# Optimization experiments

Measured on AMD Instinct MI355X. Metric: run time of the kernel, lower is better.

The kernel has to match this reference:

```python
import jax, jax.numpy as jnp
import numpy as np

B = 8192
D_IN = 1024
D_H = 1024


def _lin(x, w, b):
    # torch nn.Linear: y = x @ w.T + b, w: [out, in]
    return x @ w.T + b


def setup_inputs() -> dict:
    key = jax.random.key(0)
    ks = iter(jax.random.split(key, 64))
    s = 0.02

    def w(shape):
        return (jax.random.normal(next(ks), shape, dtype=jnp.float32) * s)

    inp = {
        "x": jax.random.normal(next(ks), (B, D_IN), dtype=jnp.float32),
        "h_prev": jax.random.normal(next(ks), (B, D_H), dtype=jnp.float32),
        "c_prev": jax.random.normal(next(ks), (B, D_H), dtype=jnp.float32),
    }
    for name in ["Wi", "Wf", "Wo", "Wc", "Ws"]:
        inp[name + "_w"] = w((D_H, D_IN))
        inp[name + "_b"] = w((D_H,))
    for name in ["Ui", "Uf", "Uo", "Uc", "Us"]:
        inp[name + "_w"] = w((D_H, D_H))
        inp[name + "_b"] = w((D_H,))
    # alpha_mlp: Linear(in+h -> h), ReLU, Linear(h -> 1), Sigmoid
    inp["a1_w"] = w((D_H, D_IN + D_H)); inp["a1_b"] = w((D_H,))
    inp["a2_w"] = w((1, D_H)); inp["a2_b"] = w((1,))
    inp["r1_w"] = w((D_H, D_H)); inp["r1_b"] = w((D_H,))
    inp["r2_w"] = w((D_H, D_H)); inp["r2_b"] = w((D_H,))
    inp["r3_w"] = w((D_H, D_H)); inp["r3_b"] = w((D_H,))
    return inp


def reference(x, h_prev, c_prev,
              Wi_w, Wi_b, Wf_w, Wf_b, Wo_w, Wo_b, Wc_w, Wc_b, Ws_w, Ws_b,
              Ui_w, Ui_b, Uf_w, Uf_b, Uo_w, Uo_b, Uc_w, Uc_b, Us_w, Us_b,
              a1_w, a1_b, a2_w, a2_b,
              r1_w, r1_b, r2_w, r2_b, r3_w, r3_b):
    i_t = jax.nn.sigmoid(_lin(x, Wi_w, Wi_b) + _lin(h_prev, Ui_w, Ui_b))
    f_t = jax.nn.sigmoid(_lin(x, Wf_w, Wf_b) + _lin(h_prev, Uf_w, Uf_b))
    o_t = jax.nn.sigmoid(_lin(x, Wo_w, Wo_b) + _lin(h_prev, Uo_w, Uo_b))
    c_hat_t = jnp.tanh(_lin(x, Wc_w, Wc_b) + _lin(h_prev, Uc_w, Uc_b))

    combined = jnp.concatenate([x, h_prev], axis=-1)  # [B, D_IN + D_H]
    alpha_t = jax.nn.sigmoid(_lin(jax.nn.relu(_lin(combined, a1_w, a1_b)), a2_w, a2_b))  # [B, 1]

    s_t = jax.nn.sigmoid(_lin(x, Ws_w, Ws_b) + _lin(h_prev, Us_w, Us_b))

    c_t = f_t * c_prev + i_t * c_hat_t * s_t * alpha_t

    residual = _lin(jax.nn.relu(_lin(jax.nn.relu(_lin(h_prev, r1_w, r1_b)), r2_w, r2_b)), r3_w, r3_b)
    c_t = c_t + residual
    h_t = o_t * jnp.tanh(c_t)
    return (h_t, c_t)
```

## Files before the change

### kernel.cpp

```cpp
#include <hip/hip_runtime.h>
#include <hip/hip_bf16.h>

typedef __bf16 bf16;
typedef __bf16 bf16x8 __attribute__((ext_vector_type(8)));
typedef __bf16 bf16x4 __attribute__((ext_vector_type(4)));
typedef float f32x4 __attribute__((ext_vector_type(4)));

#define NBIG 7168
#define KBIG 2048

__device__ __forceinline__ float sigmoid_f(float x) { return 1.0f / (1.0f + __expf(-x)); }
__device__ __forceinline__ float tanh_f(float x) { return 1.0f - 2.0f / (__expf(2.0f * x) + 1.0f); }

__device__ __forceinline__ void gload_lds16(const bf16* g, bf16* lds) {
  __builtin_amdgcn_global_load_lds(
      (const __attribute__((address_space(1))) unsigned int*)g,
      (__attribute__((address_space(3))) unsigned int*)lds,
      16, 0, 0);
}


__global__ __launch_bounds__(256) void build_A(const float* __restrict__ x,
                                               const float* __restrict__ h,
                                               bf16* __restrict__ A) {
  const int i4 = blockIdx.x * 256 + threadIdx.x;
  const int o = i4 * 4;
  const int m = o >> 11;
  const int c = o & 2047;
  const float4 v = (c < 1024) ? *(const float4*)&x[(size_t)m * 1024 + c]
                              : *(const float4*)&h[(size_t)m * 1024 + (c - 1024)];
  bf16x4 b;
  b[0] = (bf16)v.x; b[1] = (bf16)v.y; b[2] = (bf16)v.z; b[3] = (bf16)v.w;
  *(bf16x4*)&A[(size_t)o] = b;
}

__global__ __launch_bounds__(256) void build_WG(
    const float* __restrict__ Wi, const float* __restrict__ Wf, const float* __restrict__ Wo,
    const float* __restrict__ Wc, const float* __restrict__ Ws,
    const float* __restrict__ Ui, const float* __restrict__ Uf, const float* __restrict__ Uo,
    const float* __restrict__ Uc, const float* __restrict__ Us,
    const float* __restrict__ a1w, const float* __restrict__ r1w, bf16* __restrict__ WG) {
  const int i4 = blockIdx.x * 256 + threadIdx.x;
  const int o = i4 * 4;
  const int n = o >> 11;
  const int c = o & 2047;
  const int g = n >> 10;
  const int r = n & 1023;
  float4 v;
  if (g < 5) {
    const float* Wp = g == 0 ? Wi : g == 1 ? Wf : g == 2 ? Wo : g == 3 ? Wc : Ws;
    const float* Up = g == 0 ? Ui : g == 1 ? Uf : g == 2 ? Uo : g == 3 ? Uc : Us;
    v = (c < 1024) ? *(const float4*)&Wp[(size_t)r * 1024 + c]
                   : *(const float4*)&Up[(size_t)r * 1024 + (c - 1024)];
  } else if (g == 5) {
    v = *(const float4*)&a1w[(size_t)r * 2048 + c];
  } else {
    if (c < 1024) { v.x = 0.f; v.y = 0.f; v.z = 0.f; v.w = 0.f; }
    else v = *(const float4*)&r1w[(size_t)r * 1024 + (c - 1024)];
  }
  bf16x4 b;
  b[0] = (bf16)v.x; b[1] = (bf16)v.y; b[2] = (bf16)v.z; b[3] = (bf16)v.w;
  *(bf16x4*)&WG[(size_t)o] = b;
}

__global__ __launch_bounds__(256) void build_bias(
    const float* __restrict__ Wib, const float* __restrict__ Wfb, const float* __restrict__ Wob,
    const float* __restrict__ Wcb, const float* __restrict__ Wsb,
    const float* __restrict__ Uib, const float* __restrict__ Ufb, const float* __restrict__ Uob,
    const float* __restrict__ Ucb, const float* __restrict__ Usb,
    const float* __restrict__ a1b, const float* __restrict__ r1b, float* __restrict__ bias) {
  const int n = blockIdx.x * 256 + threadIdx.x;
  if (n >= NBIG) return;
  const int g = n >> 10, r = n & 1023;
  float v;
  if (g < 5) {
    const float* Wb = g == 0 ? Wib : g == 1 ? Wfb : g == 2 ? Wob : g == 3 ? Wcb : Wsb;
    const float* Ub = g == 0 ? Uib : g == 1 ? Ufb : g == 2 ? Uob : g == 3 ? Ucb : Usb;
    v = Wb[r] + Ub[r];
  } else if (g == 5) v = a1b[r];
  else v = r1b[r];
  bias[n] = v;
}

__global__ __launch_bounds__(256) void f2b(const float* __restrict__ s, bf16* __restrict__ d,
                                           int n4) {
  const int i = blockIdx.x * 256 + threadIdx.x;
  if (i >= n4) return;
  const float4 v = *(const float4*)&s[(size_t)i * 4];
  bf16x4 b;
  b[0] = (bf16)v.x; b[1] = (bf16)v.y; b[2] = (bf16)v.z; b[3] = (bf16)v.w;
  *(bf16x4*)&d[(size_t)i * 4] = b;
}

__global__ __launch_bounds__(256) void gemm_bt(const bf16* __restrict__ A, int lda,
                                               const bf16* __restrict__ W, int K,
                                               const float* __restrict__ bias,
                                               bf16* __restrict__ C, int ldc, int act_mode) {
  __shared__ __align__(16) bf16 As[128 * 32];
  __shared__ __align__(16) bf16 Bs[128 * 32];

  const int tid = threadIdx.x;
  const int lane = tid & 63;
  const int wv = tid >> 6;
  const int bm = blockIdx.x * 128;
  const int bn = blockIdx.y * 128;
  const int wr = wv >> 1, wc = wv & 1;

  const int srow = wv * 16 + (lane >> 2);
  const int scol = (lane & 3) * 8;
  const bf16* ag0 = A + (size_t)(bm + srow) * lda + scol;
  const bf16* ag1 = ag0 + (size_t)64 * lda;
  const bf16* bg0 = W + (size_t)(bn + srow) * K + scol;
  const bf16* bg1 = bg0 + (size_t)64 * K;
  bf16* const al0 = &As[(wv * 16) * 32];
  bf16* const al1 = &As[(64 + wv * 16) * 32];
  bf16* const bl0 = &Bs[(wv * 16) * 32];
  bf16* const bl1 = &Bs[(64 + wv * 16) * 32];

  f32x4 acc[4][4] = {};

  const int k0 = (lane >> 4) * 8;
  const int fr = lane & 15;
  const int niter = K >> 5;
  for (int kt = 0; kt < niter; ++kt) {
    __syncthreads();
    gload_lds16(ag0, al0);
    gload_lds16(ag1, al1);
    gload_lds16(bg0, bl0);
    gload_lds16(bg1, bl1);
    ag0 += 32; ag1 += 32; bg0 += 32; bg1 += 32;
    __syncthreads();

    bf16x8 af[4], bfv[4];
#pragma unroll
    for (int f = 0; f < 4; ++f) {
      af[f] = *(const bf16x8*)&As[(wr * 64 + f * 16 + fr) * 32 + k0];
      bfv[f] = *(const bf16x8*)&Bs[(wc * 64 + f * 16 + fr) * 32 + k0];
    }
#pragma unroll
    for (int i = 0; i < 4; ++i)
#pragma unroll
      for (int j = 0; j < 4; ++j)
        acc[i][j] = __builtin_amdgcn_mfma_f32_16x16x32_bf16(af[i], bfv[j], acc[i][j], 0, 0, 0);
  }

  const int rbase = (lane >> 4) * 4;
#pragma unroll
  for (int j = 0; j < 4; ++j) {
    const int n = bn + wc * 64 + j * 16 + fr;
    const float bv = bias[n];
    const int g = (act_mode == 0) ? (n >> 10) : (act_mode == 1 ? 100 : 101);
#pragma unroll
    for (int i = 0; i < 4; ++i) {
      const size_t mrow = (size_t)(bm + wr * 64 + i * 16 + rbase);
#pragma unroll
      for (int r = 0; r < 4; ++r) {
        float v = acc[i][j][r] + bv;
        if (g == 3) v = tanh_f(v);
        else if (g < 5) v = sigmoid_f(v);
        else if (g < 7 || g == 100) v = fmaxf(v, 0.0f);
        C[(mrow + r) * (size_t)ldc + n] = (bf16)v;
      }
    }
  }
}

__global__ __launch_bounds__(256) void alpha_k(const bf16* __restrict__ G,
                                               const float* __restrict__ a2w,
                                               const float* __restrict__ a2b,
                                               float* __restrict__ alpha) {
  const int m = blockIdx.x * 4 + (threadIdx.x >> 6);
  const int lane = threadIdx.x & 63;
  const bf16* row = G + (size_t)m * NBIG + 5120 + lane * 16;
  const bf16x8 v0 = *(const bf16x8*)row;
  const bf16x8 v1 = *(const bf16x8*)(row + 8);
  const float* w = a2w + lane * 16;
  float s = 0.f;
#pragma unroll
  for (int e = 0; e < 8; ++e) s += (float)v0[e] * w[e] + (float)v1[e] * w[8 + e];
#pragma unroll
  for (int off = 32; off > 0; off >>= 1) s += __shfl_down(s, off, 64);
  if (lane == 0) alpha[m] = sigmoid_f(s + a2b[0]);
}

__global__ __launch_bounds__(256) void final_k(const bf16* __restrict__ G,
                                               const bf16* __restrict__ R3,
                                               const float* __restrict__ c_prev,
                                               const float* __restrict__ alpha,
                                               float* __restrict__ out) {
  const int idx = blockIdx.x * 256 + threadIdx.x;
  const int o = idx * 8;
  const int m = o >> 10;
  const int c = o & 1023;
  const size_t gb = (size_t)m * NBIG;
  const bf16x8 iv = *(const bf16x8*)&G[gb + c];
  const bf16x8 fv = *(const bf16x8*)&G[gb + 1024 + c];
  const bf16x8 ov = *(const bf16x8*)&G[gb + 2048 + c];
  const bf16x8 cv = *(const bf16x8*)&G[gb + 3072 + c];
  const bf16x8 sv = *(const bf16x8*)&G[gb + 4096 + c];
  const bf16x8 rv = *(const bf16x8*)&R3[(size_t)m * 1024 + c];
  const float al = alpha[m];
  const float* cp = &c_prev[(size_t)m * 1024 + c];
  float hbuf[8], cbuf[8];
#pragma unroll
  for (int e = 0; e < 8; ++e) {
    const float ct = (float)fv[e] * cp[e] + (float)iv[e] * (float)cv[e] * (float)sv[e] * al
                     + (float)rv[e];
    cbuf[e] = ct;
    hbuf[e] = (float)ov[e] * tanh_f(ct);
  }
  float* oh = out + (size_t)m * 1024 + c;
  float* oc = out + (size_t)8192 * 1024 + (size_t)m * 1024 + c;
#pragma unroll
  for (int e = 0; e < 8; ++e) { oh[e] = hbuf[e]; oc[e] = cbuf[e]; }
}

extern "C" void kernel_launch(void* const* d_in, const int* in_sizes, int n_in,
                              void* d_out, int out_size, void* d_ws, size_t ws_size,
                              hipStream_t stream) {
  const float* x      = (const float*)d_in[0];
  const float* h_prev = (const float*)d_in[1];
  const float* c_prev = (const float*)d_in[2];
  const float* Wi_w = (const float*)d_in[3];  const float* Wi_b = (const float*)d_in[4];
  const float* Wf_w = (const float*)d_in[5];  const float* Wf_b = (const float*)d_in[6];
  const float* Wo_w = (const float*)d_in[7];  const float* Wo_b = (const float*)d_in[8];
  const float* Wc_w = (const float*)d_in[9];  const float* Wc_b = (const float*)d_in[10];
  const float* Ws_w = (const float*)d_in[11]; const float* Ws_b = (const float*)d_in[12];
  const float* Ui_w = (const float*)d_in[13]; const float* Ui_b = (const float*)d_in[14];
  const float* Uf_w = (const float*)d_in[15]; const float* Uf_b = (const float*)d_in[16];
  const float* Uo_w = (const float*)d_in[17]; const float* Uo_b = (const float*)d_in[18];
  const float* Uc_w = (const float*)d_in[19]; const float* Uc_b = (const float*)d_in[20];
  const float* Us_w = (const float*)d_in[21]; const float* Us_b = (const float*)d_in[22];
  const float* a1_w = (const float*)d_in[23]; const float* a1_b = (const float*)d_in[24];
  const float* a2_w = (const float*)d_in[25]; const float* a2_b = (const float*)d_in[26];
  const float* r1_w = (const float*)d_in[27]; const float* r1_b = (const float*)d_in[28];
  const float* r2_w = (const float*)d_in[29]; const float* r2_b = (const float*)d_in[30];
  const float* r3_w = (const float*)d_in[31]; const float* r3_b = (const float*)d_in[32];

  char* ws = (char*)d_ws;
  size_t off = 0;
  auto alloc = [&](size_t bytes) -> void* {
    void* p = ws + off;
    off += (bytes + 255) & ~(size_t)255;
    return p;
  };
  bf16* A_big    = (bf16*)alloc((size_t)8192 * 2048 * 2);
  bf16* WG       = (bf16*)alloc((size_t)7168 * 2048 * 2);
  float* bias_bg = (float*)alloc((size_t)7168 * 4);
  bf16* WR2      = (bf16*)alloc((size_t)1024 * 1024 * 2);
  bf16* WR3      = (bf16*)alloc((size_t)1024 * 1024 * 2);
  bf16* G        = (bf16*)alloc((size_t)8192 * 7168 * 2);
  bf16* R2       = (bf16*)alloc((size_t)8192 * 1024 * 2);
  bf16* R3       = (bf16*)alloc((size_t)8192 * 1024 * 2);
  float* alpha   = (float*)alloc((size_t)8192 * 4);

  build_A<<<16384, 256, 0, stream>>>(x, h_prev, A_big);
  build_WG<<<14336, 256, 0, stream>>>(Wi_w, Wf_w, Wo_w, Wc_w, Ws_w,
                                      Ui_w, Uf_w, Uo_w, Uc_w, Us_w, a1_w, r1_w, WG);
  build_bias<<<28, 256, 0, stream>>>(Wi_b, Wf_b, Wo_b, Wc_b, Ws_b,
                                     Ui_b, Uf_b, Uo_b, Uc_b, Us_b, a1_b, r1_b, bias_bg);
  f2b<<<1024, 256, 0, stream>>>(r2_w, WR2, 262144);
  f2b<<<1024, 256, 0, stream>>>(r3_w, WR3, 262144);

  dim3 g1(64, 56);
  gemm_bt<<<g1, 256, 0, stream>>>(A_big, 2048, WG, 2048, bias_bg, G, NBIG, 0);

  alpha_k<<<2048, 256, 0, stream>>>(G, a2_w, a2_b, alpha);

  dim3 g2(64, 8);
  gemm_bt<<<g2, 256, 0, stream>>>(G + 6144, NBIG, WR2, 1024, r2_b, R2, 1024, 1);
  gemm_bt<<<g2, 256, 0, stream>>>(R2, 1024, WR3, 1024, r3_b, R3, 1024, 2);

  final_k<<<4096, 256, 0, stream>>>(G, R3, c_prev, alpha, (float*)d_out);
}
```

Measured before the change: 469.9 us.

## Replace big gate GEMM with 256x256 tiled, double-buffered, swizzled MFMA kernel

Measured after the change: 537.7 us. 14.4% more time.

```diff
diff --git a/kernel.cpp b/kernel.cpp
--- a/kernel.cpp
+++ b/kernel.cpp
@@ -92,6 +92,153 @@
   *(bf16x4*)&d[(size_t)i * 4] = b;
 }
 
+
+#define BAR __builtin_amdgcn_s_barrier()
+#define LGKM0 asm volatile("s_waitcnt lgkmcnt(0)" ::: "memory")
+#define VM4 asm volatile("s_waitcnt vmcnt(4)" ::: "memory")
+#define VM0 asm volatile("s_waitcnt vmcnt(0)" ::: "memory")
+#define PRIO1 __builtin_amdgcn_s_setprio(1)
+#define PRIO0 __builtin_amdgcn_s_setprio(0)
+
+__global__ __launch_bounds__(512, 2) void gemm256(
+    const bf16* __restrict__ A, int lda,
+    const bf16* __restrict__ W, int ldw, int K,
+    const float* __restrict__ bias,
+    bf16* __restrict__ C, int ldc, int act_mode, int mtiles) {
+  __shared__ __align__(16) bf16 sA[2][256 * 64];
+  __shared__ __align__(16) bf16 sB[2][256 * 64];
+
+  const int tid = threadIdx.x;
+  const int lane = tid & 63;
+  const int wv = tid >> 6;
+  const int wr = wv >> 2;
+  const int wc = wv & 3;
+
+  const int nwg = gridDim.x;
+  int wg = blockIdx.x;
+  if ((nwg & 7) == 0) wg = (wg & 7) * (nwg >> 3) + (wg >> 3);
+  const int bm = (wg % mtiles) * 256;
+  const int bn = (wg / mtiles) * 256;
+
+  const int srow = tid >> 3;
+  const int scole = ((tid & 7) ^ (srow & 7)) << 3;
+  const bf16* pA = A + (size_t)(bm + srow) * lda + scole;
+  const bf16* pB = W + (size_t)(bn + srow) * ldw + scole;
+
+  const int fr = lane & 15;
+  const int lg = lane >> 4;
+  const int swz = (lane & 7) << 4;
+
+  const int NT = K >> 6;
+
+  f32x4 acc[8][4] = {};
+  bf16x8 ar[4][2], br0[2][2], br1[2][2];
+
+#define STG_A(bb, hh, tt)                                          \
+  do {                                                             \
+    const bf16* g_ = pA + (size_t)((hh) * 128) * lda + (tt) * 64;  \
+    bf16* l_ = &sA[bb][((hh) * 128 + wv * 8) * 64];                \
+    gload_lds16(g_, l_);                                           \
+    gload_lds16(g_ + (size_t)64 * lda, l_ + 64 * 64);              \
+  } while (0)
+#define STG_B(bb, hh, tt)                                          \
+  do {                                                             \
+    const bf16* g_ = pB + (size_t)((hh) * 128) * ldw + (tt) * 64;  \
+    bf16* l_ = &sB[bb][((hh) * 128 + wv * 8) * 64];                \
+    gload_lds16(g_, l_);                                           \
+    gload_lds16(g_ + (size_t)64 * ldw, l_ + 64 * 64);              \
+  } while (0)
+#define LD_A(bb, mlo)                                                            \
+  do {                                                                           \
+    _Pragma("unroll") for (int mi = 0; mi < 4; ++mi)                             \
+    _Pragma("unroll") for (int kk = 0; kk < 2; ++kk)                             \
+        ar[mi][kk] = *(const bf16x8*)((const char*)&sA[bb][0] +                  \
+            (wr * 128 + ((mlo) + mi) * 16 + fr) * 128 +                          \
+            ((lg * 16 + kk * 64) ^ swz));                                        \
+  } while (0)
+#define LD_B(dst, bb, nlo)                                                       \
+  do {                                                                           \
+    _Pragma("unroll") for (int ni = 0; ni < 2; ++ni)                             \
+    _Pragma("unroll") for (int kk = 0; kk < 2; ++kk)                             \
+        dst[ni][kk] = *(const bf16x8*)((const char*)&sB[bb][0] +                 \
+            (wc * 64 + ((nlo) + ni) * 16 + fr) * 128 +                           \
+            ((lg * 16 + kk * 64) ^ swz));                                        \
+  } while (0)
+#define MM(mlo, nlo, br)                                                         \
+  do {                                                                           \
+    _Pragma("unroll") for (int mi = 0; mi < 4; ++mi)                             \
+    _Pragma("unroll") for (int ni = 0; ni < 2; ++ni) {                           \
+      acc[(mlo) + mi][(nlo) + ni] = __builtin_amdgcn_mfma_f32_16x16x32_bf16(     \
+          ar[mi][0], br[ni][0], acc[(mlo) + mi][(nlo) + ni], 0, 0, 0);           \
+      acc[(mlo) + mi][(nlo) + ni] = __builtin_amdgcn_mfma_f32_16x16x32_bf16(     \
+          ar[mi][1], br[ni][1], acc[(mlo) + mi][(nlo) + ni], 0, 0, 0);           \
+    }                                                                            \
+  } while (0)
+
+  STG_A(0, 0, 0); STG_A(0, 1, 0); STG_B(0, 0, 0); STG_B(0, 1, 0);
+  STG_B(1, 0, 1); STG_B(1, 1, 1);
+  VM4; BAR;
+
+  for (int t = 0; t + 3 < NT; t += 2) {
+    LD_A(0, 0); LD_B(br0, 0, 0); STG_A(1, 0, t + 1);
+    BAR; LGKM0; PRIO1; MM(0, 0, br0); PRIO0; BAR;
+    LD_B(br1, 0, 2); STG_A(1, 1, t + 1);
+    BAR; LGKM0; PRIO1; MM(0, 2, br1); PRIO0; BAR;
+    LD_A(0, 4); STG_B(0, 0, t + 2);
+    BAR; LGKM0; PRIO1; MM(4, 2, br1); PRIO0; BAR;
+    STG_B(0, 1, t + 2);
+    BAR; PRIO1; MM(4, 0, br0); PRIO0; VM4; BAR;
+    LD_A(1, 0); LD_B(br0, 1, 0); STG_A(0, 0, t + 2);
+    BAR; LGKM0; PRIO1; MM(0, 0, br0); PRIO0; BAR;
+    LD_B(br1, 1, 2); STG_A(0, 1, t + 2);
+    BAR; LGKM0; PRIO1; MM(0, 2, br1); PRIO0; BAR;
+    LD_A(1, 4); STG_B(1, 0, t + 3);
+    BAR; LGKM0; PRIO1; MM(4, 2, br1); PRIO0; BAR;
+    STG_B(1, 1, t + 3);
+    BAR; PRIO1; MM(4, 0, br0); PRIO0; VM4; BAR;
+  }
+
+  LD_A(0, 0); LD_B(br0, 0, 0); STG_A(1, 0, NT - 1);
+  BAR; LGKM0; PRIO1; MM(0, 0, br0); PRIO0; BAR;
+  LD_B(br1, 0, 2); STG_A(1, 1, NT - 1);
+  BAR; LGKM0; PRIO1; MM(0, 2, br1); PRIO0; BAR;
+  LD_A(0, 4);
+  BAR; LGKM0; PRIO1; MM(4, 2, br1); PRIO0; BAR;
+  PRIO1; MM(4, 0, br0); PRIO0; VM0; BAR;
+  LD_A(1, 0); LD_B(br0, 1, 0);
+  BAR; LGKM0; PRIO1; MM(0, 0, br0); PRIO0; BAR;
+  LD_B(br1, 1, 2);
+  BAR; LGKM0; PRIO1; MM(0, 2, br1); PRIO0; BAR;
+  LD_A(1, 4);
+  BAR; LGKM0; PRIO1; MM(4, 2, br1); PRIO0; BAR;
+  PRIO1; MM(4, 0, br0); PRIO0;
+
+  const int rbase = lg * 4;
+#pragma unroll
+  for (int j = 0; j < 4; ++j) {
+    const int n = bn + wc * 64 + j * 16 + fr;
+    const float bv = bias[n];
+    const int g = (act_mode == 0) ? (n >> 10) : (act_mode == 1 ? 100 : 101);
+#pragma unroll
+    for (int mi = 0; mi < 8; ++mi) {
+      const size_t mrow = (size_t)(bm + wr * 128 + mi * 16 + rbase);
+#pragma unroll
+      for (int r = 0; r < 4; ++r) {
+        float v = acc[mi][j][r] + bv;
+        if (g == 3) v = tanh_f(v);
+        else if (g < 5) v = sigmoid_f(v);
+        else if (g < 7 || g == 100) v = fmaxf(v, 0.0f);
+        C[(mrow + r) * (size_t)ldc + n] = (bf16)v;
+      }
+    }
+  }
+#undef STG_A
+#undef STG_B
+#undef LD_A
+#undef LD_B
+#undef MM
+}
+
 __global__ __launch_bounds__(256) void gemm_bt(const bf16* __restrict__ A, int lda,
                                                const bf16* __restrict__ W, int K,
                                                const float* __restrict__ bias,
@@ -262,8 +409,7 @@
   f2b<<<1024, 256, 0, stream>>>(r2_w, WR2, 262144);
   f2b<<<1024, 256, 0, stream>>>(r3_w, WR3, 262144);
 
-  dim3 g1(64, 56);
-  gemm_bt<<<g1, 256, 0, stream>>>(A_big, 2048, WG, 2048, bias_bg, G, NBIG, 0);
+  gemm256<<<32 * 28, 512, 0, stream>>>(A_big, 2048, WG, 2048, 2048, bias_bg, G, NBIG, 0, 32);
 
   alpha_k<<<2048, 256, 0, stream>>>(G, a2_w, a2_b, alpha);
 
```
